# Performance work log

Measured on AMD Instinct MI355X. Metric: run time of the kernel, lower is better.

Reference implementation:

```python
import jax, jax.numpy as jnp
import numpy as np
from jax import lax

EPS = 1e-6
TANH_CLIP = 1.0 - 1e-5
FRECHET_ITERS = 10


def _sqnorm(x):
    return jnp.sum(x * x, axis=-1, keepdims=True)


def _norm(x):
    return jnp.sqrt(jnp.clip(_sqnorm(x), EPS))


def _lambda(x, c):
    # conformal factor lambda_x = 2 / (1 - c ||x||^2)
    return 2.0 / jnp.clip(1.0 - c * _sqnorm(x), EPS)


def mobius_add(x, y, c):
    x2 = _sqnorm(x)
    y2 = _sqnorm(y)
    xy = jnp.sum(x * y, axis=-1, keepdims=True)
    num = (1.0 + 2.0 * c * xy + c * y2) * x + (1.0 - c * x2) * y
    den = 1.0 + 2.0 * c * xy + (c * c) * x2 * y2
    return num / jnp.clip(den, EPS)


def expmap(x, u, c):
    sc = jnp.sqrt(c)
    un = _norm(u)
    second = jnp.tanh(sc * _lambda(x, c) * un / 2.0) * u / (sc * un)
    return mobius_add(x, second, c)


def logmap(x, y, c):
    sc = jnp.sqrt(c)
    m = mobius_add(-x, y, c)
    mn = _norm(m)
    t = jnp.arctanh(jnp.clip(sc * mn, 0.0, TANH_CLIP))
    return (2.0 / (sc * _lambda(x, c))) * t * m / mn


def exp0(u, c):
    sc = jnp.sqrt(c)
    un = _norm(u)
    return jnp.tanh(sc * un) * u / (sc * un)


def dist(x, y, c):
    sc = jnp.sqrt(c)
    mn = _norm(mobius_add(-x, y, c))
    return (2.0 / sc) * jnp.arctanh(jnp.clip(sc * mn, 0.0, TANH_CLIP))[..., 0]


def gyr(a, b, w, c):
    # gyr[a,b]w = -(a (+) b) (+) (a (+) (b (+) w))
    return mobius_add(-mobius_add(a, b, c), mobius_add(a, mobius_add(b, w, c), c), c)


def transp(x, y, u, c):
    # parallel transport x -> y:  (lam_x / lam_y) * gyr[y, -x] u
    return (_lambda(x, c) / _lambda(y, c)) * gyr(y, -x, u, c)


def frechet_mean(x, c):
    # Karcher fixed-point iteration: mu <- exp_mu(mean_i log_mu(x_i))
    m = jnp.mean(x, axis=0)  # (D,)
    max_norm = (1.0 - 1e-3) / jnp.sqrt(c)
    mn = _norm(m)[0]
    m = m * jnp.minimum(1.0, max_norm / mn)

    def step(mu, _):
        g = jnp.mean(logmap(mu, x, c), axis=0)
        return expmap(mu, g, c), None

    mu, _ = lax.scan(step, m, None, length=FRECHET_ITERS)
    return mu


def setup_inputs() -> dict:
    key = jax.random.key(0)
    k1, k2 = jax.random.split(key)
    B, S, D = 64, 256, 256
    K = jnp.float32(-1.2)
    sc = np.sqrt(1.2)
    x = jax.random.normal(k1, (B, S, D), dtype=jnp.float32)
    # project points strictly inside the Poincare ball of radius 1/sqrt(c)
    x = x / (1.0 + _norm(x)) * jnp.float32(0.7 / sc)
    mean_param = 0.01 * jax.random.normal(k2, (D,), dtype=jnp.float32)
    var_param = jnp.float32(1.0)
    return {"x": x, "K": K, "mean_param": mean_param, "var_param": var_param}


def reference(x, K, mean_param, var_param):
    c = -K  # positive ball curvature (K = -1.2)
    shapes = x.shape
    xf = x.reshape(-1, shapes[-1])  # (N, D)
    on_manifold = exp0(mean_param, c)          # (D,) target mean on manifold
    mu = frechet_mean(xf, c)                   # (D,) batch Frechet mean
    var = jnp.mean(dist(xf, mu, c) ** 2)       # Frechet variance (scalar)
    logm = transp(mu, on_manifold, logmap(mu, xf, c), c)  # (N, D)
    logm = jnp.sqrt(var_param / (var + 1e-6)) * logm
    out = expmap(on_manifold, logm, c)         # (N, D)
    return out.reshape(shapes)
```

## Files before the change

### kernel.cpp

```cpp
#include <hip/hip_runtime.h>
#include <math.h>
#include <string.h>

#define EPSF 1e-6f
#define TCLIP (1.0f - 1e-5f)
#define NPTS 16384
#define DDIM 256
#define NBLK 128
#define NTHR 1024
#define PPB 128
#define NWAVE 16
#define PPW 8
#define PSTR 260
#define FRECHET_ITERS_N 10

#define WS_BAR 0
#define WS_PA 64
#define WS_PB (WS_PA + NBLK * PSTR)

__device__ __forceinline__ void st_pair_sc1(float* addr, float a, float b) {
    float2 f2 = make_float2(a, b);
    double dv; memcpy(&dv, &f2, 8);
    __hip_atomic_store((double*)addr, dv, __ATOMIC_RELAXED, __HIP_MEMORY_SCOPE_AGENT);
}
__device__ __forceinline__ float2 ld_pair_sc1(const float* addr) {
    double dv = __hip_atomic_load((const double*)addr, __ATOMIC_RELAXED, __HIP_MEMORY_SCOPE_AGENT);
    float2 f2; memcpy(&f2, &dv, 8);
    return f2;
}
__device__ __forceinline__ void st_f_sc1(float* addr, float v) {
    __hip_atomic_store(addr, v, __ATOMIC_RELAXED, __HIP_MEMORY_SCOPE_AGENT);
}
__device__ __forceinline__ float ld_f_sc1(const float* addr) {
    return __hip_atomic_load(addr, __ATOMIC_RELAXED, __HIP_MEMORY_SCOPE_AGENT);
}

__device__ __forceinline__ float block_sum(float v) {
    __shared__ float s_bs[NWAVE];
    #pragma unroll
    for (int off = 32; off; off >>= 1) v += __shfl_xor(v, off);
    const int w = threadIdx.x >> 6, l = threadIdx.x & 63;
    __syncthreads();
    if (l == 0) s_bs[w] = v;
    __syncthreads();
    float s = 0.f;
    #pragma unroll
    for (int i = 0; i < NWAVE; ++i) s += s_bs[i];
    return s;
}

__device__ __forceinline__ void gbar(unsigned* cnt, unsigned target) {
    __syncthreads();
    if (threadIdx.x == 0) {
        __hip_atomic_fetch_add(cnt, 1u, __ATOMIC_RELAXED, __HIP_MEMORY_SCOPE_AGENT);
        while (__hip_atomic_load(cnt, __ATOMIC_RELAXED, __HIP_MEMORY_SCOPE_AGENT) < target)
            __builtin_amdgcn_s_sleep(1);
    }
    __syncthreads();
}

__global__ void init_bar(float* ws) { ((unsigned*)(ws + WS_BAR))[0] = 0u; }

__global__ __launch_bounds__(NTHR, 1) void rbn_fused(
    const float* __restrict__ x, const float* __restrict__ Kp,
    const float* __restrict__ mean_param, const float* __restrict__ var_param,
    float* __restrict__ out, float* __restrict__ ws)
{
    const float c = -Kp[0];
    const float sc = sqrtf(c);
    const int t = threadIdx.x, lane = t & 63, wv = t >> 6;
    const int b = blockIdx.x;
    const int p0 = b * PPB;
    const float4* xr = ((const float4*)x) + p0 * 64;

    unsigned* bar = (unsigned*)(ws + WS_BAR);
    float* PA = ws + WS_PA;
    float* PB = ws + WS_PB;

    __shared__ float mu_s[DDIM], om_s[DDIM], g_s[DDIM];
    __shared__ float dpart[PPB * 65];
    __shared__ float dqr[PPB * 9];
    __shared__ float y2_s[PPB], e_s[PPB], d_s[PPB], w_s[PPB], sA_s[PPB], fx_s[PPB];
    __shared__ float pseg[NWAVE * DDIM];

    unsigned barno = 0;

    float4 xreg[PPW];
    #pragma unroll
    for (int i = 0; i < PPW; ++i)
        xreg[i] = xr[(wv * PPW + i) * 64 + lane];

    auto dot_rows = [&](float4 v4, float* dst, bool self) {
        __syncthreads();
        #pragma unroll
        for (int i = 0; i < PPW; ++i) {
            float4 xv = xreg[i];
            float4 u4 = self ? xv : v4;
            dpart[(wv * PPW + i) * 65 + lane] =
                xv.x * u4.x + xv.y * u4.y + xv.z * u4.z + xv.w * u4.w;
        }
        __syncthreads();
        {
            int pl = t & 127, q = t >> 7;
            float s = 0.f;
            #pragma unroll
            for (int j = 0; j < 8; ++j) s += dpart[pl * 65 + q * 8 + j];
            dqr[pl * 9 + q] = s;
        }
        __syncthreads();
        if (t < PPB) {
            float s = 0.f;
            #pragma unroll
            for (int j = 0; j < 8; ++j) s += dqr[t * 9 + j];
            dst[t] = s;
        }
        __syncthreads();
    };

    auto wsum_rows = [&](const float* wgt, float* dstv) {
        float4 a = make_float4(0.f, 0.f, 0.f, 0.f);
        #pragma unroll
        for (int i = 0; i < PPW; ++i) {
            float w = wgt ? wgt[wv * PPW + i] : 1.f;
            a.x += w * xreg[i].x; a.y += w * xreg[i].y;
            a.z += w * xreg[i].z; a.w += w * xreg[i].w;
        }
        __syncthreads();
        ((float4*)(pseg + wv * DDIM))[lane] = a;
        __syncthreads();
        float s = 0.f;
        if (t < DDIM) {
            #pragma unroll
            for (int w = 0; w < NWAVE; ++w) s += pseg[w * DDIM + t];
        }
        float partner = __shfl_xor(s, 1);
        if (t < DDIM && !(t & 1))
            st_pair_sc1(dstv + t, s, partner);
    };

    auto reduce128 = [&](const float* buf, float* dstv) {
        const int dg = t & 127, sg = t >> 7;
        float ax = 0.f, ay = 0.f;
        #pragma unroll
        for (int j = 0; j < 16; ++j) {
            float2 v = ld_pair_sc1(buf + (sg * 16 + j) * PSTR + 2 * dg);
            ax += v.x; ay += v.y;
        }
        __syncthreads();
        ((float2*)(pseg + sg * DDIM))[dg] = make_float2(ax, ay);
        __syncthreads();
        if (t < DDIM) {
            float s = 0.f;
            #pragma unroll
            for (int w = 0; w < 8; ++w) s += pseg[w * DDIM + t];
            dstv[t] = s;
        }
        __syncthreads();
    };

    {
        float u = (t < DDIM) ? mean_param[t] : 0.f;
        float un2 = block_sum(u * u);
        float un = sqrtf(fmaxf(un2, EPSF));
        if (t < DDIM) om_s[t] = tanhf(sc * un) * u / (sc * un);
    }
    float om2;
    { float v = (t < DDIM) ? om_s[t] * om_s[t] : 0.f; om2 = block_sum(v); }

    dot_rows(make_float4(0.f, 0.f, 0.f, 0.f), y2_s, true);
    {
        float4 om4 = ((const float4*)om_s)[lane];
        dot_rows(om4, e_s, false);
    }

    wsum_rows(nullptr, PA + b * PSTR);
    gbar(bar, ++barno * NBLK);

    float mu2;
    {
        reduce128(PA, g_s);
        float m = (t < DDIM) ? g_s[t] * (1.f / NPTS) : 0.f;
        float mn2 = block_sum(m * m);
        float mn = sqrtf(fmaxf(mn2, EPSF));
        float maxn = (1.f - 1e-3f) / sc;
        float f = fminf(1.f, maxn / mn);
        if (t < DDIM) mu_s[t] = m * f;
        float v = (m * f) * (m * f);
        mu2 = block_sum(v);
    }

    for (int it = 0; it < FRECHET_ITERS_N; ++it) {
        float* buf = (it & 1) ? PA : PB;
        {
            float4 mu4 = ((const float4*)mu_s)[lane];
            dot_rows(mu4, d_s, false);
        }
        if (t < PPB) {
            float y2 = y2_s[t], d = d_s[t];
            float P = 1.f - 2.f * c * d;
            float den = fmaxf(P + c * c * mu2 * y2, EPSF);
            float A = -(P + c * y2) / den;
            float B = (1.f - c * mu2) / den;
            float mn2 = fmaxf(A * A * mu2 + 2.f * A * B * d + B * B * y2, EPSF);
            float mn = sqrtf(mn2);
            float tt = atanhf(fminf(sc * mn, TCLIP));
            float s = (fmaxf(1.f - c * mu2, EPSF) / sc) * tt / mn;
            w_s[t] = s * B;
            sA_s[t] = s * A;
        }
        __syncthreads();
        wsum_rows(w_s, buf + b * PSTR);
        float sAv = (t < PPB) ? sA_s[t] : 0.f;
        float sAtot = block_sum(sAv);
        if (t == 0) st_f_sc1(buf + b * PSTR + DDIM, sAtot);
        gbar(bar, ++barno * NBLK);

        reduce128(buf, g_s);
        float sa = (t < NBLK) ? ld_f_sc1(buf + t * PSTR + DDIM) : 0.f;
        float sAt = block_sum(sa);
        float mu = (t < DDIM) ? mu_s[t] : 0.f;
        float g = (t < DDIM) ? g_s[t] * (1.f / NPTS) + (sAt * (1.f / NPTS)) * mu : 0.f;
        float gn2 = block_sum(g * g);
        float mg  = block_sum(mu * g);
        float un = sqrtf(fmaxf(gn2, EPSF));
        float lam = 2.f / fmaxf(1.f - c * mu2, EPSF);
        float k = tanhf(sc * lam * un * 0.5f) / (sc * un);
        float sec = k * g;
        float ms = k * mg;
        float s2 = k * k * gn2;
        float aa = 1.f + 2.f * c * ms + c * s2;
        float bb2 = 1.f - c * mu2;
        float den = fmaxf(1.f + 2.f * c * ms + c * c * mu2 * s2, EPSF);
        float nmu = (aa * mu + bb2 * sec) / den;
        if (t < DDIM) mu_s[t] = nmu;
        float v2 = (t < DDIM) ? nmu * nmu : 0.f;
        mu2 = block_sum(v2);
    }

    float* vbuf = ((FRECHET_ITERS_N - 1) & 1) ? PB : PA;
    {
        float4 mu4 = ((const float4*)mu_s)[lane];
        dot_rows(mu4, d_s, false);
    }
    if (t < PPB) {
        float y2 = y2_s[t], d = d_s[t];
        float P = 1.f - 2.f * c * d;
        float den = fmaxf(P + c * c * mu2 * y2, EPSF);
        float A = -(P + c * y2) / den;
        float B = (1.f - c * mu2) / den;
        float mn2 = fmaxf(A * A * mu2 + 2.f * A * B * d + B * B * y2, EPSF);
        float mn = sqrtf(mn2);
        float tt = atanhf(fminf(sc * mn, TCLIP));
        float dd = (2.f / sc) * tt;
        sA_s[t] = dd * dd;
    }
    __syncthreads();
    {
        float v = (t < PPB) ? sA_s[t] : 0.f;
        float tot = block_sum(v);
        if (t == 0) st_f_sc1(vbuf + b * PSTR + DDIM, tot);
    }
    gbar(bar, ++barno * NBLK);

    float var, gamma;
    {
        float sa = (t < NBLK) ? ld_f_sc1(vbuf + t * PSTR + DDIM) : 0.f;
        var = block_sum(sa) * (1.f / NPTS);
        gamma = sqrtf(var_param[0] / (var + 1e-6f));
    }

    float omu;
    {
        float muv = (t < DDIM) ? mu_s[t] : 0.f;
        float omv = (t < DDIM) ? om_s[t] : 0.f;
        omu = block_sum(omv * muv);
    }
    const float Amu = fmaxf(1.f - c * mu2, EPSF);
    const float Aom = fmaxf(1.f - c * om2, EPSF);
    const float ratio = Aom / Amu;
    const float aq = 1.f - 2.f * c * omu + c * mu2;
    const float bq = 1.f - c * om2;
    const float dqv = fmaxf(1.f - 2.f * c * omu + c * c * om2 * mu2, EPSF);
    const float qo = aq / dqv, qm = -bq / dqv;
    const float q2 = qo * qo * om2 + 2.f * qo * qm * omu + qm * qm * mu2;
    const float lam_om = 2.f / Aom;

    if (t < PPB) {
        float y2 = y2_s[t], d = d_s[t], e = e_s[t];
        auto dotOm3 = [&](float po, float pm, float px) { return po * om2 + pm * omu + px * e; };
        auto dotMu3 = [&](float po, float pm, float px) { return po * omu + pm * mu2 + px * d; };
        auto sqn3 = [&](float po, float pm, float px) {
            return po * po * om2 + pm * pm * mu2 + px * px * y2
                 + 2.f * (po * pm * omu + po * px * e + pm * px * d);
        };

        float P = 1.f - 2.f * c * d;
        float den0 = fmaxf(P + c * c * mu2 * y2, EPSF);
        float A = -(P + c * y2) / den0;
        float B = (1.f - c * mu2) / den0;
        float mn2 = fmaxf(A * A * mu2 + 2.f * A * B * d + B * B * y2, EPSF);
        float mn = sqrtf(mn2);
        float tt = atanhf(fminf(sc * mn, TCLIP));
        float s = (fmaxf(1.f - c * mu2, EPSF) / sc) * tt / mn;
        float Um = s * A, Ux = s * B;

        float xy1 = -dotMu3(0.f, Um, Ux);
        float Y21 = sqn3(0.f, Um, Ux);
        float a1 = 1.f + 2.f * c * xy1 + c * Y21;
        float b1 = 1.f - c * mu2;
        float dn1 = fmaxf(1.f + 2.f * c * xy1 + c * c * mu2 * Y21, EPSF);
        float h1m = (-a1 + b1 * Um) / dn1;
        float h1x = (b1 * Ux) / dn1;

        float xy2 = dotOm3(0.f, h1m, h1x);
        float Y22 = sqn3(0.f, h1m, h1x);
        float a2 = 1.f + 2.f * c * xy2 + c * Y22;
        float b2 = 1.f - c * om2;
        float dn2 = fmaxf(1.f + 2.f * c * xy2 + c * c * om2 * Y22, EPSF);
        float h2o = a2 / dn2;
        float h2m = (b2 * h1m) / dn2;
        float h2x = (b2 * h1x) / dn2;

        float xy3 = -(qo * dotOm3(h2o, h2m, h2x) + qm * dotMu3(h2o, h2m, h2x));
        float Y23 = sqn3(h2o, h2m, h2x);
        float a3 = 1.f + 2.f * c * xy3 + c * Y23;
        float b3 = 1.f - c * q2;
        float dn3 = fmaxf(1.f + 2.f * c * xy3 + c * c * q2 * Y23, EPSF);
        float g2o = (-a3 * qo + b3 * h2o) / dn3;
        float g2m = (-a3 * qm + b3 * h2m) / dn3;
        float g2x = (b3 * h2x) / dn3;

        float k1 = ratio * gamma;
        float Lo = k1 * g2o, Lm = k1 * g2m, Lx = k1 * g2x;
        float un2 = sqn3(Lo, Lm, Lx);
        float un = sqrtf(fmaxf(un2, EPSF));
        float coef = tanhf(sc * lam_om * un * 0.5f) / (sc * un);
        float So = coef * Lo, Sm = coef * Lm, Sx = coef * Lx;
        float xy4 = dotOm3(So, Sm, Sx);
        float Y24 = coef * coef * un2;
        float a4 = 1.f + 2.f * c * xy4 + c * Y24;
        float b4 = 1.f - c * om2;
        float dn4 = fmaxf(1.f + 2.f * c * xy4 + c * c * om2 * Y24, EPSF);
        w_s[t]  = (a4 + b4 * So) / dn4;
        sA_s[t] = (b4 * Sm) / dn4;
        fx_s[t] = (b4 * Sx) / dn4;
    }
    __syncthreads();

    {
        float4 mu4f = ((const float4*)mu_s)[lane];
        float4 om4f = ((const float4*)om_s)[lane];
        #pragma unroll
        for (int i = 0; i < PPW; ++i) {
            int pl = wv * PPW + i;
            float fo = w_s[pl], fm = sA_s[pl], fx = fx_s[pl];
            float4 x4 = xreg[i];
            float4 o4;
            o4.x = fo * om4f.x + fm * mu4f.x + fx * x4.x;
            o4.y = fo * om4f.y + fm * mu4f.y + fx * x4.y;
            o4.z = fo * om4f.z + fm * mu4f.z + fx * x4.z;
            o4.w = fo * om4f.w + fm * mu4f.w + fx * x4.w;
            ((float4*)out)[(p0 + pl) * 64 + lane] = o4;
        }
    }
}

extern "C" void kernel_launch(void* const* d_in, const int* in_sizes, int n_in,
                              void* d_out, int out_size, void* d_ws, size_t ws_size,
                              hipStream_t stream) {
    const float* x = (const float*)d_in[0];
    const float* K = (const float*)d_in[1];
    const float* mean_param = (const float*)d_in[2];
    const float* var_param = (const float*)d_in[3];
    float* out = (float*)d_out;
    float* ws = (float*)d_ws;

    init_bar<<<1, 1, 0, stream>>>(ws);
    void* args[] = {(void*)&x, (void*)&K, (void*)&mean_param, (void*)&var_param,
                    (void*)&out, (void*)&ws};
    hipLaunchCooperativeKernel((const void*)rbn_fused, dim3(NBLK), dim3(NTHR),
                               args, 0, stream);
}
```

Measured before the change: 206.9 us.

## Replace counter grid barrier with per-block tags and fuse block reductions

After: 207.1 us. About the same (+0.1%).

```diff
diff --git a/kernel.cpp b/kernel.cpp
--- a/kernel.cpp
+++ b/kernel.cpp
@@ -14,7 +14,6 @@
 #define PSTR 260
 #define FRECHET_ITERS_N 10
 
-#define WS_BAR 0
 #define WS_PA 64
 #define WS_PB (WS_PA + NBLK * PSTR)
 
@@ -31,7 +30,10 @@
 __device__ __forceinline__ void st_f_sc1(float* addr, float v) {
     __hip_atomic_store(addr, v, __ATOMIC_RELAXED, __HIP_MEMORY_SCOPE_AGENT);
 }
-__device__ __forceinline__ float ld_f_sc1(const float* addr) {
+__device__ __forceinline__ void st_u_sc1(unsigned* addr, unsigned v) {
+    __hip_atomic_store(addr, v, __ATOMIC_RELAXED, __HIP_MEMORY_SCOPE_AGENT);
+}
+__device__ __forceinline__ unsigned ld_u_sc1(const unsigned* addr) {
     return __hip_atomic_load(addr, __ATOMIC_RELAXED, __HIP_MEMORY_SCOPE_AGENT);
 }
 
@@ -49,17 +51,41 @@
     return s;
 }
 
-__device__ __forceinline__ void gbar(unsigned* cnt, unsigned target) {
-    __syncthreads();
-    if (threadIdx.x == 0) {
-        __hip_atomic_fetch_add(cnt, 1u, __ATOMIC_RELAXED, __HIP_MEMORY_SCOPE_AGENT);
-        while (__hip_atomic_load(cnt, __ATOMIC_RELAXED, __HIP_MEMORY_SCOPE_AGENT) < target)
-            __builtin_amdgcn_s_sleep(1);
-    }
-    __syncthreads();
-}
-
-__global__ void init_bar(float* ws) { ((unsigned*)(ws + WS_BAR))[0] = 0u; }
+__device__ __forceinline__ void block_sum2(float& a, float& b) {
+    __shared__ float sa2[NWAVE], sb2[NWAVE];
+    #pragma unroll
+    for (int off = 32; off; off >>= 1) { a += __shfl_xor(a, off); b += __shfl_xor(b, off); }
+    const int w = threadIdx.x >> 6, l = threadIdx.x & 63;
+    __syncthreads();
+    if (l == 0) { sa2[w] = a; sb2[w] = b; }
+    __syncthreads();
+    a = 0.f; b = 0.f;
+    #pragma unroll
+    for (int i = 0; i < NWAVE; ++i) { a += sa2[i]; b += sb2[i]; }
+}
+
+__device__ __forceinline__ void block_sum3(float& a, float& b, float& cc) {
+    __shared__ float sa3[NWAVE], sb3[NWAVE], sc3[NWAVE];
+    #pragma unroll
+    for (int off = 32; off; off >>= 1) {
+        a += __shfl_xor(a, off); b += __shfl_xor(b, off); cc += __shfl_xor(cc, off);
+    }
+    const int w = threadIdx.x >> 6, l = threadIdx.x & 63;
+    __syncthreads();
+    if (l == 0) { sa3[w] = a; sb3[w] = b; sc3[w] = cc; }
+    __syncthreads();
+    a = 0.f; b = 0.f; cc = 0.f;
+    #pragma unroll
+    for (int i = 0; i < NWAVE; ++i) { a += sa3[i]; b += sb3[i]; cc += sc3[i]; }
+}
+
+__global__ void init_tags(float* ws) {
+    int t = threadIdx.x;
+    if (t < NBLK) {
+        st_u_sc1((unsigned*)(ws + WS_PA + t * PSTR + 258), 0u);
+        st_u_sc1((unsigned*)(ws + WS_PB + t * PSTR + 258), 0u);
+    }
+}
 
 __global__ __launch_bounds__(NTHR, 1) void rbn_fused(
     const float* __restrict__ x, const float* __restrict__ Kp,
@@ -68,12 +94,12 @@
 {
     const float c = -Kp[0];
     const float sc = sqrtf(c);
+    const float N1 = 1.f / NPTS;
     const int t = threadIdx.x, lane = t & 63, wv = t >> 6;
     const int b = blockIdx.x;
     const int p0 = b * PPB;
     const float4* xr = ((const float4*)x) + p0 * 64;
 
-    unsigned* bar = (unsigned*)(ws + WS_BAR);
     float* PA = ws + WS_PA;
     float* PB = ws + WS_PB;
 
@@ -91,7 +117,6 @@
         xreg[i] = xr[(wv * PPW + i) * 64 + lane];
 
     auto dot_rows = [&](float4 v4, float* dst, bool self) {
-        __syncthreads();
         #pragma unroll
         for (int i = 0; i < PPW; ++i) {
             float4 xv = xreg[i];
@@ -138,6 +163,18 @@
             st_pair_sc1(dstv + t, s, partner);
     };
 
+    auto publish = [&](float* buf) {
+        __syncthreads();
+        if (t == 0) st_u_sc1((unsigned*)(buf + b * PSTR + 258), barno);
+    };
+    auto wait_tags = [&](const float* buf) {
+        if (t < NBLK) {
+            const unsigned* tg = (const unsigned*)(buf + t * PSTR + 258);
+            while (ld_u_sc1(tg) < barno) {}
+        }
+        __syncthreads();
+    };
+
     auto reduce128 = [&](const float* buf, float* dstv) {
         const int dg = t & 127, sg = t >> 7;
         float ax = 0.f, ay = 0.f;
@@ -173,24 +210,27 @@
         dot_rows(om4, e_s, false);
     }
 
+    ++barno;
     wsum_rows(nullptr, PA + b * PSTR);
-    gbar(bar, ++barno * NBLK);
+    publish(PA);
+    wait_tags(PA);
 
     float mu2;
     {
         reduce128(PA, g_s);
-        float m = (t < DDIM) ? g_s[t] * (1.f / NPTS) : 0.f;
+        float m = (t < DDIM) ? g_s[t] * N1 : 0.f;
         float mn2 = block_sum(m * m);
         float mn = sqrtf(fmaxf(mn2, EPSF));
         float maxn = (1.f - 1e-3f) / sc;
         float f = fminf(1.f, maxn / mn);
         if (t < DDIM) mu_s[t] = m * f;
-        float v = (m * f) * (m * f);
-        mu2 = block_sum(v);
+        mu2 = f * f * mn2;
+        __syncthreads();
     }
 
     for (int it = 0; it < FRECHET_ITERS_N; ++it) {
         float* buf = (it & 1) ? PA : PB;
+        ++barno;
         {
             float4 mu4 = ((const float4*)mu_s)[lane];
             dot_rows(mu4, d_s, false);
@@ -210,34 +250,38 @@
         }
         __syncthreads();
         wsum_rows(w_s, buf + b * PSTR);
-        float sAv = (t < PPB) ? sA_s[t] : 0.f;
-        float sAtot = block_sum(sAv);
-        if (t == 0) st_f_sc1(buf + b * PSTR + DDIM, sAtot);
-        gbar(bar, ++barno * NBLK);
+        float sAl = (t < PPB) ? sA_s[t] : 0.f;
+        float wdl = (t < PPB) ? w_s[t] * d_s[t] : 0.f;
+        block_sum2(sAl, wdl);
+        if (t == 0) st_pair_sc1(buf + b * PSTR + 256, sAl, wdl);
+        publish(buf);
+        wait_tags(buf);
 
         reduce128(buf, g_s);
-        float sa = (t < NBLK) ? ld_f_sc1(buf + t * PSTR + DDIM) : 0.f;
-        float sAt = block_sum(sa);
-        float mu = (t < DDIM) ? mu_s[t] : 0.f;
-        float g = (t < DDIM) ? g_s[t] * (1.f / NPTS) + (sAt * (1.f / NPTS)) * mu : 0.f;
-        float gn2 = block_sum(g * g);
-        float mg  = block_sum(mu * g);
+        float vv  = (t < DDIM) ? g_s[t] * g_s[t] : 0.f;
+        float2 sp = make_float2(0.f, 0.f);
+        if (t < NBLK) sp = ld_pair_sc1(buf + t * PSTR + 256);
+        float sAt = sp.x, wdt = sp.y;
+        block_sum3(vv, sAt, wdt);
+        float gn2 = N1 * N1 * (vv + 2.f * sAt * wdt + sAt * sAt * mu2);
+        float mg  = N1 * (wdt + sAt * mu2);
         float un = sqrtf(fmaxf(gn2, EPSF));
         float lam = 2.f / fmaxf(1.f - c * mu2, EPSF);
         float k = tanhf(sc * lam * un * 0.5f) / (sc * un);
-        float sec = k * g;
         float ms = k * mg;
         float s2 = k * k * gn2;
         float aa = 1.f + 2.f * c * ms + c * s2;
         float bb2 = 1.f - c * mu2;
         float den = fmaxf(1.f + 2.f * c * ms + c * c * mu2 * s2, EPSF);
-        float nmu = (aa * mu + bb2 * sec) / den;
-        if (t < DDIM) mu_s[t] = nmu;
-        float v2 = (t < DDIM) ? nmu * nmu : 0.f;
-        mu2 = block_sum(v2);
+        float cm = (aa + bb2 * k * N1 * sAt) / den;
+        float cv = (bb2 * k * N1) / den;
+        if (t < DDIM) mu_s[t] = cm * mu_s[t] + cv * g_s[t];
+        mu2 = cm * cm * mu2 + 2.f * cm * cv * wdt + cv * cv * vv;
+        __syncthreads();
     }
 
     float* vbuf = ((FRECHET_ITERS_N - 1) & 1) ? PB : PA;
+    ++barno;
     {
         float4 mu4 = ((const float4*)mu_s)[lane];
         dot_rows(mu4, d_s, false);
@@ -258,23 +302,19 @@
     {
         float v = (t < PPB) ? sA_s[t] : 0.f;
         float tot = block_sum(v);
-        if (t == 0) st_f_sc1(vbuf + b * PSTR + DDIM, tot);
-    }
-    gbar(bar, ++barno * NBLK);
-
-    float var, gamma;
-    {
-        float sa = (t < NBLK) ? ld_f_sc1(vbuf + t * PSTR + DDIM) : 0.f;
-        var = block_sum(sa) * (1.f / NPTS);
-        gamma = sqrtf(var_param[0] / (var + 1e-6f));
-    }
-
-    float omu;
-    {
-        float muv = (t < DDIM) ? mu_s[t] : 0.f;
-        float omv = (t < DDIM) ? om_s[t] : 0.f;
-        omu = block_sum(omv * muv);
-    }
+        if (t == 0) st_f_sc1(vbuf + b * PSTR + 256, tot);
+    }
+    publish(vbuf);
+    wait_tags(vbuf);
+
+    float va = (t < NBLK) ? __hip_atomic_load(vbuf + t * PSTR + 256,
+                 __ATOMIC_RELAXED, __HIP_MEMORY_SCOPE_AGENT) : 0.f;
+    float ob = (t < DDIM) ? om_s[t] * mu_s[t] : 0.f;
+    block_sum2(va, ob);
+    float var = va * N1;
+    float gamma = sqrtf(var_param[0] / (var + 1e-6f));
+    float omu = ob;
+
     const float Amu = fmaxf(1.f - c * mu2, EPSF);
     const float Aom = fmaxf(1.f - c * om2, EPSF);
     const float ratio = Aom / Amu;
@@ -375,7 +415,7 @@
     float* out = (float*)d_out;
     float* ws = (float*)d_ws;
 
-    init_bar<<<1, 1, 0, stream>>>(ws);
+    init_tags<<<1, 256, 0, stream>>>(ws);
     void* args[] = {(void*)&x, (void*)&K, (void*)&mean_param, (void*)&var_param,
                     (void*)&out, (void*)&ws};
     hipLaunchCooperativeKernel((const void*)rbn_fused, dim3(NBLK), dim3(NTHR),
```
